# Performance work log

Hardware: AMD Instinct MI355X
Metric: run time of the kernel (lower is better)

The kernel has to match this reference:

```python
import jax, jax.numpy as jnp
import numpy as np
import math

D = 256; NH = 8; NG = 64; META = 6

def _linear(x, w, b):
    return x @ w.T + b

def setup_inputs():
    key = jax.random.key(0)
    ks = jax.random.split(key, 12)
    B, T, TG = 32, 4096, 1024
    def rn(k, shape, s=0.02):
        return jax.random.normal(k, shape, dtype=jnp.float32) * s
    q = jax.random.normal(ks[0], (1, NG, D), dtype=jnp.float32)
    q = q / jnp.clip(jnp.linalg.norm(q, axis=-1, keepdims=True), 1e-6)
    # fibonacci unit sphere anchor, scaled by 0.4
    idx = jnp.arange(NG, dtype=jnp.float32)
    golden = (1.0 + math.sqrt(5.0)) / 2.0
    theta = 2.0 * math.pi * idx / golden
    z = jnp.clip(1.0 - (2.0 * idx + 1.0) / NG, -1.0 + 1e-6, 1.0 - 1e-6)
    r = jnp.sqrt(jnp.clip(1.0 - z * z, 0.0))
    pts = jnp.stack([r * jnp.cos(theta), r * jnp.sin(theta), z], axis=-1)
    pts = pts / jnp.clip(jnp.linalg.norm(pts, axis=-1, keepdims=True), 1e-6)
    p0 = (pts * 0.4)[None]
    ph_b2 = jnp.array([0.0] * 6 + [-2.0] * 4, dtype=jnp.float32)
    return dict(
        local_feat=jax.random.normal(ks[1], (B, D, T), dtype=jnp.float32),
        global_feat=jax.random.normal(ks[2], (B, D, TG), dtype=jnp.float32),
        meta=jax.random.uniform(ks[3], (B, META), dtype=jnp.float32),
        queries=q, p0_anchor=p0,
        in_proj_w=rn(ks[4], (3 * D, D)), in_proj_b=jnp.zeros((3 * D,), jnp.float32),
        out_proj_w=rn(ks[5], (D, D)), out_proj_b=jnp.zeros((D,), jnp.float32),
        ln_g=jnp.ones((D,), jnp.float32), ln_b=jnp.zeros((D,), jnp.float32),
        meta_w=rn(ks[6], (D, META)), meta_b=jnp.zeros((D,), jnp.float32),
        temporal_w=rn(ks[7], (D, D)), temporal_b=jnp.zeros((D,), jnp.float32),
        shift_w=rn(ks[8], (3, D)), shift_b=jnp.zeros((3,), jnp.float32),
        ph_w1=rn(ks[9], (D // 2, D)), ph_b1=jnp.zeros((D // 2,), jnp.float32),
        ph_w2=rn(ks[10], (10, D // 2)), ph_b2=ph_b2,
        wave_delay_scale=jnp.float32(0.1),
        envelope_bias=jnp.float32(0.5),
    )

def reference(local_feat, global_feat, meta, queries, p0_anchor, in_proj_w, in_proj_b,
              out_proj_w, out_proj_b, ln_g, ln_b, meta_w, meta_b, temporal_w, temporal_b,
              shift_w, shift_b, ph_w1, ph_b1, ph_w2, ph_b2, wave_delay_scale, envelope_bias):
    B, _, T = local_feat.shape
    DH = D // NH
    kv = jnp.transpose(global_feat, (0, 2, 1))                        # [B,TG,D]
    q = jnp.broadcast_to(queries, (B, NG, D))
    wq, wk, wv = in_proj_w[:D], in_proj_w[D:2 * D], in_proj_w[2 * D:]
    bq, bk, bv = in_proj_b[:D], in_proj_b[D:2 * D], in_proj_b[2 * D:]
    qh = _linear(q, wq, bq).reshape(B, NG, NH, DH)
    kh = _linear(kv, wk, bk).reshape(B, -1, NH, DH)
    vh = _linear(kv, wv, bv).reshape(B, -1, NH, DH)
    attn = jax.nn.softmax(jnp.einsum('bqhd,bkhd->bhqk', qh, kh) / math.sqrt(DH), axis=-1)
    ctx = jnp.einsum('bhqk,bkhd->bqhd', attn, vh).reshape(B, NG, D)
    x = q + _linear(ctx, out_proj_w, out_proj_b)
    mu = x.mean(-1, keepdims=True)
    var = ((x - mu) ** 2).mean(-1, keepdims=True)
    q_static = (x - mu) / jnp.sqrt(var + 1e-5) * ln_g + ln_b
    q_static = q_static + jax.nn.gelu(_linear(meta, meta_w, meta_b), approximate=False)[:, None, :]
    params = _linear(jax.nn.gelu(_linear(q_static, ph_w1, ph_b1), approximate=False), ph_w2, ph_b2)
    p0_delta = jnp.tanh(params[..., 0:3]) * 0.2
    heart_shift = jnp.tanh(_linear(global_feat.mean(-1), shift_w, shift_b)) * 0.3
    p_pos = p0_anchor + p0_delta + heart_shift[:, None, :]            # [B,NG,3]
    dnorm = jnp.clip(jnp.linalg.norm(params[..., 3:6], axis=-1, keepdims=True), 1e-6)
    dipole_dir = params[..., 3:6] / dnorm
    volume_xyz = jax.nn.sigmoid(params[..., 6:9]) * 0.5 + 0.001
    amplitude = jax.nn.sigmoid(params[..., 9]) + 1e-4                 # [B,NG]
    tw = _linear(q_static, temporal_w, temporal_b)                    # [B,NG,D]
    temporal_logits = jnp.einsum('bnc,bct->bnt', tw, local_feat) / math.sqrt(D)
    idx_sa = jnp.argmax(amplitude, axis=1)                            # [B]
    p_sa = jnp.take_along_axis(p_pos, idx_sa[:, None, None], axis=1)  # [B,1,3]
    dist = jnp.linalg.norm(p_pos - p_sa, axis=-1)                     # [B,NG]
    delay = jnp.clip(jax.nn.softplus(wave_delay_scale) * dist, 0.0, 0.1)
    base_x = jnp.linspace(-1.0, 1.0, T)
    grid_x = base_x[None, None, :] - delay[..., None]                 # [B,NG,T]
    # grid_sample(bilinear, zeros, align_corners=True): grid_y hits rows exactly,
    # so it reduces to 1D linear interp along time with zero padding.
    x_pix = (grid_x + 1.0) * 0.5 * (T - 1)
    x0 = jnp.floor(x_pix).astype(jnp.int32)
    x1 = x0 + 1
    w1 = x_pix - x0.astype(x_pix.dtype)
    w0 = 1.0 - w1
    def samp(xi):
        g = jnp.take_along_axis(temporal_logits, jnp.clip(xi, 0, T - 1), axis=-1)
        return g * ((xi >= 0) & (xi <= T - 1)).astype(g.dtype)
    shifted = w0 * samp(x0) + w1 * samp(x1)
    envelope_t = jax.nn.sigmoid(shifted + envelope_bias)              # [B,NG,T]
    return amplitude, p_pos, dipole_dir, volume_xyz, envelope_t
```

## Files before the change

### kernel.cpp

```cpp
#include <hip/hip_runtime.h>
#include <hip/hip_bf16.h>
#include <math.h>

typedef __hip_bfloat16 bf16;
typedef short s16x8 __attribute__((ext_vector_type(8)));
typedef float f32x4 __attribute__((ext_vector_type(4)));

#define NDIM 256
#define NTG 1024
#define NT 4096

__device__ __forceinline__ float gelu_exact(float x) {
    return 0.5f * x * (1.0f + erff(x * 0.70710678118654752440f));
}
__device__ __forceinline__ float sigmoidf_(float x) {
    return 1.0f / (1.0f + __expf(-x));
}
__device__ __forceinline__ short f2bf_s(float x) {
    union { bf16 h; short s; } cv;
    cv.h = __float2bfloat16(x);
    return cv.s;
}
__device__ __forceinline__ float bf2f(short s) {
    union { bf16 h; short s; } cv;
    cv.s = s;
    return __bfloat162float(cv.h);
}

__global__ __launch_bounds__(256) void k_prep(
        const float* __restrict__ gf, const float* __restrict__ ipw,
        const float* __restrict__ opw, const float* __restrict__ twm,
        const float* __restrict__ pw1, const float* __restrict__ queries,
        const float* __restrict__ ipb,
        bf16* __restrict__ gfT, float* __restrict__ partial,
        float* __restrict__ opwT, float* __restrict__ twT, float* __restrict__ pw1T,
        bf16* __restrict__ wkvK, bf16* __restrict__ wkvV,
        float* __restrict__ qh) {
    __shared__ float smem[64 * 65 + 256];
    int blk = blockIdx.x, tid = threadIdx.x;
    if (blk < 2048) {
        float (*tile)[65] = (float(*)[65])smem;
        float* psum = smem + 64 * 65;
        int t0 = (blk & 15) * 64, c0 = ((blk >> 4) & 3) * 64, b = blk >> 6;
        int tt = tid & 63, ci = tid >> 6;
        #pragma unroll
        for (int r = 0; r < 16; ++r) {
            int cl = ci * 16 + r;
            tile[cl][tt] = gf[((size_t)(b * 256 + c0 + cl)) * NTG + t0 + tt];
        }
        __syncthreads();
        int cc = tid & 63, ti = tid >> 6;
        #pragma unroll
        for (int r = 0; r < 16; ++r) {
            int tl = ti * 16 + r;
            gfT[((size_t)(b * 1024 + t0 + tl)) * 256 + c0 + cc] =
                __float2bfloat16(tile[cc][tl]);
        }
        float ps = 0.f;
        #pragma unroll
        for (int r = 0; r < 16; ++r) ps += tile[cc][ti * 16 + r];
        psum[tid] = ps;
        __syncthreads();
        if (tid < 64) {
            float s = psum[tid] + psum[tid + 64] + psum[tid + 128] + psum[tid + 192];
            partial[(b * 256 + c0 + tid) * 16 + (blk & 15)] = s;
        }
    } else {
        int pblk = blk - 2048;
        if (pblk < 384) {
            int id = pblk * 256 + tid;
            if (id < 65536) {
                int k = id >> 8, c = id & 255;
                opwT[id] = opw[c * 256 + k];
                twT[id]  = twm[c * 256 + k];
            } else {
                int id2 = id - 65536;
                int k = id2 >> 7, m = id2 & 127;
                pw1T[id2] = pw1[m * 256 + k];
            }
        } else if (pblk < 640) {
            int id = (pblk - 384) * 256 + tid;
            wkvK[id] = __float2bfloat16(ipw[65536 + id]);
            wkvV[id] = __float2bfloat16(ipw[131072 + id]);
        } else {
            float* qrow = smem;
            int n = pblk - 640, c = tid;
            qrow[c] = queries[n * 256 + c];
            __syncthreads();
            float s = ipb[c];
            const float* wr = ipw + c * 256;
            for (int k = 0; k < 256; ++k) s += qrow[k] * wr[k];
            qh[n * 256 + c] = s;
        }
    }
}

__global__ __launch_bounds__(256) void k_kv(
        const short* __restrict__ gfT, const short* __restrict__ wkvK,
        const short* __restrict__ wkvV, const float* __restrict__ ipb,
        const float* __restrict__ meta, const float* __restrict__ mw,
        const float* __restrict__ mb, const float* __restrict__ partial,
        const float* __restrict__ sw, const float* __restrict__ sb,
        short* __restrict__ kvh, short* __restrict__ vTg,
        float* __restrict__ metag, float* __restrict__ hshift) {
    int blk = blockIdx.x;
    int tid = threadIdx.x;
    if (blk >= 2048) {
        __shared__ float gm[256];
        int b = blk - 2048, c = tid;
        float m = 0.f;
        const float* pp = partial + (b * 256 + c) * 16;
        #pragma unroll
        for (int tt = 0; tt < 16; ++tt) m += pp[tt];
        gm[c] = m * (1.0f / 1024.0f);
        float s = mb[c];
        #pragma unroll
        for (int j = 0; j < 6; ++j) s += meta[b * 6 + j] * mw[c * 6 + j];
        metag[b * 256 + c] = gelu_exact(s);
        __syncthreads();
        if (c < 3) {
            float t = sb[c];
            for (int k = 0; k < 256; ++k) t += gm[k] * sw[c * 256 + k];
            hshift[b * 4 + c] = tanhf(t) * 0.3f;
        }
        return;
    }
    int w = tid >> 6, lane = tid & 63, lm = lane & 15, quad = lane >> 4;
    int bx = blk & 7, byq = (blk >> 3) & 7, b = blk >> 6;
    int t0 = bx * 128 + w * 32;
    int sel = byq >> 2;
    int n0 = (byq & 3) * 64;
    if (sel == 0) {
        f32x4 acc[4][2];
        #pragma unroll
        for (int ni = 0; ni < 4; ++ni)
            #pragma unroll
            for (int mt = 0; mt < 2; ++mt) acc[ni][mt] = (f32x4)(0.0f);
        #pragma unroll
        for (int ks = 0; ks < 8; ++ks) {
            int c = ks * 32 + quad * 8;
            s16x8 bg[2];
            #pragma unroll
            for (int mt = 0; mt < 2; ++mt)
                bg[mt] = *(const s16x8*)&gfT[((size_t)(b * 1024 + t0 + mt * 16 + lm)) * 256 + c];
            #pragma unroll
            for (int ni = 0; ni < 4; ++ni) {
                s16x8 aw = *(const s16x8*)&wkvK[(n0 + ni * 16 + lm) * 256 + c];
                #pragma unroll
                for (int mt = 0; mt < 2; ++mt)
                    acc[ni][mt] = __builtin_amdgcn_mfma_f32_16x16x32_bf16(aw, bg[mt], acc[ni][mt], 0, 0, 0);
            }
        }
        #pragma unroll
        for (int ni = 0; ni < 4; ++ni) {
            int nb4 = n0 + ni * 16 + quad * 4;
            float4 bias = *(const float4*)&ipb[256 + nb4];
            #pragma unroll
            for (int mt = 0; mt < 2; ++mt) {
                int t = t0 + mt * 16 + lm;
                ushort4 o;
                o.x = (unsigned short)f2bf_s(acc[ni][mt][0] + bias.x);
                o.y = (unsigned short)f2bf_s(acc[ni][mt][1] + bias.y);
                o.z = (unsigned short)f2bf_s(acc[ni][mt][2] + bias.z);
                o.w = (unsigned short)f2bf_s(acc[ni][mt][3] + bias.w);
                *(ushort4*)&kvh[((size_t)(b * 1024 + t)) * 256 + nb4] = o;
            }
        }
    } else {
        f32x4 acc[2][4];
        #pragma unroll
        for (int mt = 0; mt < 2; ++mt)
            #pragma unroll
            for (int ni = 0; ni < 4; ++ni) acc[mt][ni] = (f32x4)(0.0f);
        #pragma unroll
        for (int ks = 0; ks < 8; ++ks) {
            int c = ks * 32 + quad * 8;
            s16x8 ag[2];
            #pragma unroll
            for (int mt = 0; mt < 2; ++mt)
                ag[mt] = *(const s16x8*)&gfT[((size_t)(b * 1024 + t0 + mt * 16 + lm)) * 256 + c];
            #pragma unroll
            for (int ni = 0; ni < 4; ++ni) {
                s16x8 bw = *(const s16x8*)&wkvV[(n0 + ni * 16 + lm) * 256 + c];
                #pragma unroll
                for (int mt = 0; mt < 2; ++mt)
                    acc[mt][ni] = __builtin_amdgcn_mfma_f32_16x16x32_bf16(ag[mt], bw, acc[mt][ni], 0, 0, 0);
            }
        }
        #pragma unroll
        for (int ni = 0; ni < 4; ++ni) {
            int nv = n0 + ni * 16 + lm;
            float bias = ipb[512 + nv];
            #pragma unroll
            for (int mt = 0; mt < 2; ++mt) {
                int t4 = t0 + mt * 16 + quad * 4;
                ushort4 o;
                o.x = (unsigned short)f2bf_s(acc[mt][ni][0] + bias);
                o.y = (unsigned short)f2bf_s(acc[mt][ni][1] + bias);
                o.z = (unsigned short)f2bf_s(acc[mt][ni][2] + bias);
                o.w = (unsigned short)f2bf_s(acc[mt][ni][3] + bias);
                *(ushort4*)&vTg[((size_t)(b * 256 + nv)) * 1024 + t4] = o;
            }
        }
    }
}

__global__ __launch_bounds__(256) void k_attn(
        const short* __restrict__ kvh, const short* __restrict__ vTg,
        const float* __restrict__ qh,
        float* __restrict__ o_half, float* __restrict__ l_half) {
    __shared__ short pT[4][64 * 40];
    __shared__ float obuf[4][64 * 36];
    __shared__ float lbuf[4 * 64];
    int tid = threadIdx.x;
    int w = tid >> 6, lane = tid & 63, lm = lane & 15, quad = lane >> 4;
    int half = blockIdx.x, h = blockIdx.y, b = blockIdx.z;
    s16x8 aq[4];
    #pragma unroll
    for (int mt = 0; mt < 4; ++mt) {
        const float* qp = qh + (mt * 16 + lm) * 256 + h * 32 + quad * 8;
        #pragma unroll
        for (int j = 0; j < 8; ++j) aq[mt][j] = f2bf_s(qp[j]);
    }
    f32x4 acco[2][4];
    #pragma unroll
    for (int dt = 0; dt < 2; ++dt)
        #pragma unroll
        for (int qt = 0; qt < 4; ++qt) acco[dt][qt] = (f32x4)(0.0f);
    float lp[4][4];
    #pragma unroll
    for (int mt = 0; mt < 4; ++mt)
        #pragma unroll
        for (int r = 0; r < 4; ++r) lp[mt][r] = 0.f;
    const float scale = 0.17677669529663687f;
    int kb = half * 512 + w * 128;
    for (int ch = 0; ch < 4; ++ch) {
        int n0 = kb + ch * 32;
        #pragma unroll
        for (int nt = 0; nt < 2; ++nt) {
            int key = n0 + nt * 16 + lm;
            s16x8 bk = *(const s16x8*)&kvh[((size_t)(b * 1024 + key)) * 256 + h * 32 + quad * 8];
            f32x4 zero = {0.f, 0.f, 0.f, 0.f};
            #pragma unroll
            for (int mt = 0; mt < 4; ++mt) {
                f32x4 S = __builtin_amdgcn_mfma_f32_16x16x32_bf16(aq[mt], bk, zero, 0, 0, 0);
                #pragma unroll
                for (int r = 0; r < 4; ++r) {
                    float e = __expf(S[r] * scale);
                    lp[mt][r] += e;
                    pT[w][(mt * 16 + quad * 4 + r) * 40 + nt * 16 + lm] = f2bf_s(e);
                }
            }
        }
        s16x8 av[2], bp[4];
        #pragma unroll
        for (int dt = 0; dt < 2; ++dt)
            av[dt] = *(const s16x8*)&vTg[((size_t)(b * 256 + h * 32 + dt * 16 + lm)) * 1024 + n0 + quad * 8];
        #pragma unroll
        for (int qt = 0; qt < 4; ++qt)
            bp[qt] = *(const s16x8*)&pT[w][(qt * 16 + lm) * 40 + quad * 8];
        #pragma unroll
        for (int dt = 0; dt < 2; ++dt)
            #pragma unroll
            for (int qt = 0; qt < 4; ++qt)
                acco[dt][qt] = __builtin_amdgcn_mfma_f32_16x16x32_bf16(av[dt], bp[qt], acco[dt][qt], 0, 0, 0);
    }
    #pragma unroll
    for (int mt = 0; mt < 4; ++mt)
        #pragma unroll
        for (int r = 0; r < 4; ++r) {
            float v = lp[mt][r];
            v += __shfl_xor(v, 1); v += __shfl_xor(v, 2);
            v += __shfl_xor(v, 4); v += __shfl_xor(v, 8);
            lp[mt][r] = v;
        }
    #pragma unroll
    for (int dt = 0; dt < 2; ++dt)
        #pragma unroll
        for (int qt = 0; qt < 4; ++qt) {
            int q = qt * 16 + lm;
            float4 t;
            t.x = acco[dt][qt][0]; t.y = acco[dt][qt][1];
            t.z = acco[dt][qt][2]; t.w = acco[dt][qt][3];
            *(float4*)&obuf[w][q * 36 + dt * 16 + quad * 4] = t;
        }
    if (lm == 0) {
        #pragma unroll
        for (int mt = 0; mt < 4; ++mt)
            #pragma unroll
            for (int r = 0; r < 4; ++r)
                lbuf[w * 64 + mt * 16 + quad * 4 + r] = lp[mt][r];
    }
    __syncthreads();
    int q = tid & 63, dg = tid >> 6;
    int blk = (b * 8 + h) * 2 + half;
    float l = lbuf[q] + lbuf[64 + q] + lbuf[128 + q] + lbuf[192 + q];
    float o[8];
    #pragma unroll
    for (int j = 0; j < 8; ++j) o[j] = 0.f;
    #pragma unroll
    for (int w2 = 0; w2 < 4; ++w2) {
        const float* src = &obuf[w2][q * 36 + dg * 8];
        #pragma unroll
        for (int j = 0; j < 8; ++j) o[j] += src[j];
    }
    float* dst = &o_half[(((size_t)blk * 64) + q) * 32 + dg * 8];
    #pragma unroll
    for (int j = 0; j < 8; ++j) dst[j] = o[j];
    if (dg == 0) l_half[blk * 64 + q] = l;
}

__global__ __launch_bounds__(256) void k_post(
        const float* __restrict__ o_half, const float* __restrict__ l_half,
        const float* __restrict__ queries,
        const float* __restrict__ opwT, const float* __restrict__ opb,
        const float* __restrict__ lng, const float* __restrict__ lnb,
        const float* __restrict__ metag, const float* __restrict__ hshift,
        const float* __restrict__ twT, const float* __restrict__ tbv,
        const float* __restrict__ pw1T, const float* __restrict__ pb1,
        const float* __restrict__ pw2, const float* __restrict__ pb2,
        const float* __restrict__ p0a,
        bf16* __restrict__ twbf, float* __restrict__ out_amp,
        float* __restrict__ out_ppos, float* __restrict__ out_dip,
        float* __restrict__ out_vol) {
    __shared__ float cs[4][256];
    __shared__ float xs[4][256];
    __shared__ float qs[4][256];
    __shared__ float h1[4][128];
    __shared__ float ps[4][10];
    int tid = threadIdx.x;
    int n0 = blockIdx.x * 4, b = blockIdx.y;
    {
        int h = tid >> 5, d = tid & 31;
        int blk0 = (b * 8 + h) * 2;
        #pragma unroll
        for (int r = 0; r < 4; ++r) {
            int q = n0 + r;
            float l = l_half[blk0 * 64 + q] + l_half[(blk0 + 1) * 64 + q];
            float v0 = o_half[(((size_t)blk0 * 64) + q) * 32 + d];
            float v1 = o_half[(((size_t)(blk0 + 1) * 64) + q) * 32 + d];
            cs[r][tid] = (v0 + v1) / l;
        }
    }
    __syncthreads();
    {
        int c = tid;
        float a[4];
        #pragma unroll
        for (int nn = 0; nn < 4; ++nn) a[nn] = opb[c];
        for (int k = 0; k < 256; ++k) {
            float w = opwT[k * 256 + c];
            #pragma unroll
            for (int nn = 0; nn < 4; ++nn) a[nn] += cs[nn][k] * w;
        }
        #pragma unroll
        for (int nn = 0; nn < 4; ++nn)
            xs[nn][c] = queries[(n0 + nn) * 256 + c] + a[nn];
    }
    __syncthreads();
    {
        int w = tid >> 6, lane = tid & 63;
        int nr = w;
        float x0 = xs[nr][lane], x1 = xs[nr][lane + 64],
              x2 = xs[nr][lane + 128], x3 = xs[nr][lane + 192];
        float s = x0 + x1 + x2 + x3;
        #pragma unroll
        for (int off = 32; off >= 1; off >>= 1) s += __shfl_xor(s, off);
        float mu = s * (1.0f / 256.0f);
        float e0 = x0 - mu, e1 = x1 - mu, e2 = x2 - mu, e3 = x3 - mu;
        float v = e0*e0 + e1*e1 + e2*e2 + e3*e3;
        #pragma unroll
        for (int off = 32; off >= 1; off >>= 1) v += __shfl_xor(v, off);
        float rstd = 1.0f / sqrtf(v * (1.0f / 256.0f) + 1e-5f);
        #pragma unroll
        for (int j = 0; j < 4; ++j) {
            int c = lane + 64 * j;
            qs[nr][c] = (xs[nr][c] - mu) * rstd * lng[c] + lnb[c] + metag[b * 256 + c];
        }
    }
    __syncthreads();
    {
        int c = tid;
        float a[4];
        #pragma unroll
        for (int nn = 0; nn < 4; ++nn) a[nn] = tbv[c];
        for (int k = 0; k < 256; ++k) {
            float w = twT[k * 256 + c];
            #pragma unroll
            for (int nn = 0; nn < 4; ++nn) a[nn] += qs[nn][k] * w;
        }
        #pragma unroll
        for (int nn = 0; nn < 4; ++nn)
            twbf[(size_t)(b * 64 + n0 + nn) * 256 + c] = __float2bfloat16(a[nn]);
    }
    {
        int m = tid & 127, g = tid >> 7;
        float a[2];
        #pragma unroll
        for (int q2 = 0; q2 < 2; ++q2) a[q2] = pb1[m];
        for (int k = 0; k < 256; ++k) {
            float w = pw1T[k * 128 + m];
            #pragma unroll
            for (int q2 = 0; q2 < 2; ++q2) a[q2] += qs[g * 2 + q2][k] * w;
        }
        #pragma unroll
        for (int q2 = 0; q2 < 2; ++q2) h1[g * 2 + q2][m] = gelu_exact(a[q2]);
    }
    __syncthreads();
    if (tid < 40) {
        int nr = tid / 10, j = tid % 10;
        float s = pb2[j];
        for (int m = 0; m < 128; ++m) s += h1[nr][m] * pw2[j * 128 + m];
        ps[nr][j] = s;
    }
    __syncthreads();
    if (tid < 4) {
        int nr = tid;
        int gn = b * 64 + n0 + nr;
        #pragma unroll
        for (int j = 0; j < 3; ++j) {
            float delta = tanhf(ps[nr][j]) * 0.2f;
            out_ppos[gn * 3 + j] = p0a[(n0 + nr) * 3 + j] + delta + hshift[b * 4 + j];
        }
        float d0 = ps[nr][3], d1 = ps[nr][4], d2 = ps[nr][5];
        float dn = fmaxf(sqrtf(d0 * d0 + d1 * d1 + d2 * d2), 1e-6f);
        out_dip[gn * 3 + 0] = d0 / dn;
        out_dip[gn * 3 + 1] = d1 / dn;
        out_dip[gn * 3 + 2] = d2 / dn;
        #pragma unroll
        for (int j = 0; j < 3; ++j)
            out_vol[gn * 3 + j] = sigmoidf_(ps[nr][6 + j]) * 0.5f + 0.001f;
        out_amp[gn] = sigmoidf_(ps[nr][9]) + 0.0001f;
    }
}

__global__ __launch_bounds__(256) void k_temporal(
        const float* __restrict__ lf, const short* __restrict__ twbf,
        short* __restrict__ logits) {
    __shared__ __align__(16) short tws[64 * 264];
    __shared__ __align__(16) short lfs[2][32 * 132];
    int tid = threadIdx.x;
    int t0 = blockIdx.x * 128, b = blockIdx.y;
    int wave = tid >> 6, lane = tid & 63;
    int lm = lane & 15, quad = lane >> 4;

    #pragma unroll
    for (int i = 0; i < 8; ++i) {
        int id = i * 256 + tid;
        int n = id >> 5, c8 = id & 31;
        s16x8 v = *(const s16x8*)&twbf[(size_t)(b * 64 + n) * 256 + c8 * 8];
        *(s16x8*)&tws[n * 264 + c8 * 8] = v;
    }

    float4 fr[4];
    #pragma unroll
    for (int r = 0; r < 4; ++r) {
        int id = r * 256 + tid;
        int c = id >> 5, t4 = id & 31;
        fr[r] = *(const float4*)&lf[((size_t)(b * 256 + c)) * 4096 + t0 + t4 * 4];
    }
    #pragma unroll
    for (int r = 0; r < 4; ++r) {
        int id = r * 256 + tid;
        int c = id >> 5, t4 = id & 31;
        ushort4 o;
        o.x = (unsigned short)f2bf_s(fr[r].x);
        o.y = (unsigned short)f2bf_s(fr[r].y);
        o.z = (unsigned short)f2bf_s(fr[r].z);
        o.w = (unsigned short)f2bf_s(fr[r].w);
        *(ushort4*)&lfs[0][c * 132 + t4 * 4] = o;
    }

    f32x4 acc[2][4];
    #pragma unroll
    for (int mi = 0; mi < 2; ++mi)
        #pragma unroll
        for (int ni = 0; ni < 4; ++ni) acc[mi][ni] = (f32x4)(0.0f);

    __syncthreads();

    for (int ksi = 0; ksi < 8; ++ksi) {
        int cur = ksi & 1;
        if (ksi < 7) {
            int c0n = (ksi + 1) * 32;
            #pragma unroll
            for (int r = 0; r < 4; ++r) {
                int id = r * 256 + tid;
                int c = id >> 5, t4 = id & 31;
                fr[r] = *(const float4*)&lf[((size_t)(b * 256 + c0n + c)) * 4096 + t0 + t4 * 4];
            }
        }
        int c0 = ksi * 32;
        #pragma unroll
        for (int mi = 0; mi < 2; ++mi) {
            int tl = wave * 32 + mi * 16 + lm;
            s16x8 af;
            #pragma unroll
            for (int j = 0; j < 8; ++j)
                af[j] = lfs[cur][(quad * 8 + j) * 132 + tl];
            #pragma unroll
            for (int ni = 0; ni < 4; ++ni) {
                s16x8 bfr = *(const s16x8*)&tws[(ni * 16 + lm) * 264 + c0 + quad * 8];
                acc[mi][ni] = __builtin_amdgcn_mfma_f32_16x16x32_bf16(af, bfr, acc[mi][ni], 0, 0, 0);
            }
        }
        if (ksi < 7) {
            #pragma unroll
            for (int r = 0; r < 4; ++r) {
                int id = r * 256 + tid;
                int c = id >> 5, t4 = id & 31;
                ushort4 o;
                o.x = (unsigned short)f2bf_s(fr[r].x);
                o.y = (unsigned short)f2bf_s(fr[r].y);
                o.z = (unsigned short)f2bf_s(fr[r].z);
                o.w = (unsigned short)f2bf_s(fr[r].w);
                *(ushort4*)&lfs[cur ^ 1][c * 132 + t4 * 4] = o;
            }
        }
        __syncthreads();
    }
    #pragma unroll
    for (int mi = 0; mi < 2; ++mi) {
        #pragma unroll
        for (int ni = 0; ni < 4; ++ni) {
            int n = ni * 16 + lm;
            int t = t0 + wave * 32 + mi * 16 + quad * 4;
            ushort4 o;
            o.x = (unsigned short)f2bf_s(acc[mi][ni][0] * 0.0625f);
            o.y = (unsigned short)f2bf_s(acc[mi][ni][1] * 0.0625f);
            o.z = (unsigned short)f2bf_s(acc[mi][ni][2] * 0.0625f);
            o.w = (unsigned short)f2bf_s(acc[mi][ni][3] * 0.0625f);
            *(ushort4*)&logits[(size_t)(b * 64 + n) * 4096 + t] = o;
        }
    }
}

__global__ void k_envelope(const short* __restrict__ logits,
                           const float* __restrict__ out_amp,
                           const float* __restrict__ out_ppos,
                           const float* __restrict__ wds,
                           const float* __restrict__ ebp,
                           float* __restrict__ env) {
    int blk = blockIdx.x;
    int bn = blk >> 2, seg = blk & 3;
    int b = bn >> 6, n = bn & 63;
    int tid = threadIdx.x;
    int lane = tid & 63;
    float v = out_amp[b * 64 + lane];
    int idx = lane;
    #pragma unroll
    for (int off = 1; off < 64; off <<= 1) {
        float ov = __shfl_xor(v, off);
        int oi = __shfl_xor(idx, off);
        if (ov > v || (ov == v && oi < idx)) { v = ov; idx = oi; }
    }
    float dx = out_ppos[(b * 64 + n) * 3 + 0] - out_ppos[(b * 64 + idx) * 3 + 0];
    float dy = out_ppos[(b * 64 + n) * 3 + 1] - out_ppos[(b * 64 + idx) * 3 + 1];
    float dz = out_ppos[(b * 64 + n) * 3 + 2] - out_ppos[(b * 64 + idx) * 3 + 2];
    float dist = sqrtf(dx * dx + dy * dy + dz * dz);
    float sp = log1pf(expf(wds[0]));
    float dl = fminf(fmaxf(sp * dist, 0.f), 0.1f);
    float eb = ebp[0];
    const short* gl = logits + (size_t)bn * 4096;
    int t_base = seg * 1024 + tid * 4;
    float ov4[4];
    #pragma unroll
    for (int u = 0; u < 4; ++u) {
        int t = t_base + u;
        float xb = fmaf((float)t, 2.0f / 4095.0f, -1.0f);
        float xp = (xb - dl + 1.0f) * 2047.5f;
        float x0f = floorf(xp);
        int x0 = (int)x0f;
        float w1 = xp - x0f, w0 = 1.0f - w1;
        float g0 = (x0 >= 0 && x0 <= 4095) ? bf2f(gl[x0]) : 0.f;
        int x1 = x0 + 1;
        float g1 = (x1 >= 0 && x1 <= 4095) ? bf2f(gl[x1]) : 0.f;
        float sh = w0 * g0 + w1 * g1;
        ov4[u] = 1.0f / (1.0f + __expf(-(sh + eb)));
    }
    float4 o; o.x = ov4[0]; o.y = ov4[1]; o.z = ov4[2]; o.w = ov4[3];
    *reinterpret_cast<float4*>(&env[(size_t)bn * 4096 + t_base]) = o;
}

extern "C" void kernel_launch(void* const* d_in, const int* in_sizes, int n_in,
                              void* d_out, int out_size, void* d_ws, size_t ws_size,
                              hipStream_t stream) {
    const float* lf   = (const float*)d_in[0];
    const float* gf   = (const float*)d_in[1];
    const float* meta = (const float*)d_in[2];
    const float* qrs  = (const float*)d_in[3];
    const float* p0a  = (const float*)d_in[4];
    const float* ipw  = (const float*)d_in[5];
    const float* ipb  = (const float*)d_in[6];
    const float* opw  = (const float*)d_in[7];
    const float* opb  = (const float*)d_in[8];
    const float* lng  = (const float*)d_in[9];
    const float* lnb  = (const float*)d_in[10];
    const float* mw   = (const float*)d_in[11];
    const float* mb   = (const float*)d_in[12];
    const float* twm  = (const float*)d_in[13];
    const float* tbv  = (const float*)d_in[14];
    const float* sw   = (const float*)d_in[15];
    const float* sb   = (const float*)d_in[16];
    const float* pw1  = (const float*)d_in[17];
    const float* pb1  = (const float*)d_in[18];
    const float* pw2  = (const float*)d_in[19];
    const float* pb2  = (const float*)d_in[20];
    const float* wds  = (const float*)d_in[21];
    const float* ebp  = (const float*)d_in[22];

    char* ws = (char*)d_ws;
    short* kvh    = (short*)(ws);
    short* vTg    = (short*)(ws + 16777216);
    short* gfT    = (short*)(ws + 33554432);
    short* logits = (short*)(ws + 50331648);
    float* o_half = (float*)(ws + 67108864);
    float* l_half = (float*)(ws + 71303168);
    short* twbf   = (short*)(ws + 71434240);
    float* qh     = (float*)(ws + 72482816);
    float* metag  = (float*)(ws + 72581120);
    float* hshift = (float*)(ws + 72613888);
    float* opwT   = (float*)(ws + 72614400);
    float* twT    = (float*)(ws + 72876544);
    float* pw1T   = (float*)(ws + 73138688);
    short* wkvK   = (short*)(ws + 73269760);
    short* wkvV   = (short*)(ws + 73400832);
    float* partial= (float*)(ws + 73531904);

    float* out_amp  = (float*)d_out;
    float* out_ppos = out_amp + 2048;
    float* out_dip  = out_amp + 8192;
    float* out_vol  = out_amp + 14336;
    float* env      = out_amp + 20480;

    k_prep<<<2752, 256, 0, stream>>>(gf, ipw, opw, twm, pw1, qrs, ipb,
                                     (bf16*)gfT, partial, opwT, twT, pw1T,
                                     (bf16*)wkvK, (bf16*)wkvV, qh);
    k_kv<<<2080, 256, 0, stream>>>(gfT, wkvK, wkvV, ipb, meta, mw, mb, partial,
                                   sw, sb, kvh, vTg, metag, hshift);
    k_attn<<<dim3(2, 8, 32), 256, 0, stream>>>(kvh, vTg, qh, o_half, l_half);
    k_post<<<dim3(16, 32), 256, 0, stream>>>(o_half, l_half, qrs, opwT, opb, lng, lnb,
                                             metag, hshift, twT, tbv, pw1T, pb1, pw2, pb2,
                                             p0a, (bf16*)twbf, out_amp, out_ppos,
                                             out_dip, out_vol);
    k_temporal<<<dim3(32, 32), 256, 0, stream>>>(lf, twbf, logits);
    k_envelope<<<8192, 256, 0, stream>>>(logits, out_amp, out_ppos, wds, ebp, env);
}
```

Before: 401.8 us.

## Reuse gfT registers across output tiles in k_kv and stage logits in LDS for envelope

k_kv now loads each block's 128x256 slice of gfT into registers once and loops over all four 64-column output tiles, cutting its grid from 2080 to 544 blocks and removing four-fold redundant activation loads. k_envelope now handles a whole (b,n) row per block: it stages the 4096 bf16 logits in zero-padded shared memory, drops the bounds checks on the gathers, and reuses the argmax/delay computation across four segments. The attention kernel's query load is vectorised to float4. Tradeoffs are higher register pressure in k_kv (16 s16x8 operands held live) and fewer blocks, which lowers parallelism.

```diff
diff --git a/kernel.cpp b/kernel.cpp
--- a/kernel.cpp
+++ b/kernel.cpp
@@ -105,9 +105,9 @@
         float* __restrict__ metag, float* __restrict__ hshift) {
     int blk = blockIdx.x;
     int tid = threadIdx.x;
-    if (blk >= 2048) {
+    if (blk >= 512) {
         __shared__ float gm[256];
-        int b = blk - 2048, c = tid;
+        int b = blk - 512, c = tid;
         float m = 0.f;
         const float* pp = partial + (b * 256 + c) * 16;
         #pragma unroll
@@ -126,80 +126,84 @@
         return;
     }
     int w = tid >> 6, lane = tid & 63, lm = lane & 15, quad = lane >> 4;
-    int bx = blk & 7, byq = (blk >> 3) & 7, b = blk >> 6;
+    int bx = blk & 7, sel = (blk >> 3) & 1, b = blk >> 4;
     int t0 = bx * 128 + w * 32;
-    int sel = byq >> 2;
-    int n0 = (byq & 3) * 64;
+    s16x8 g[8][2];
+    #pragma unroll
+    for (int ks = 0; ks < 8; ++ks) {
+        int c = ks * 32 + quad * 8;
+        #pragma unroll
+        for (int mt = 0; mt < 2; ++mt)
+            g[ks][mt] = *(const s16x8*)&gfT[((size_t)(b * 1024 + t0 + mt * 16 + lm)) * 256 + c];
+    }
     if (sel == 0) {
-        f32x4 acc[4][2];
-        #pragma unroll
-        for (int ni = 0; ni < 4; ++ni)
-            #pragma unroll
-            for (int mt = 0; mt < 2; ++mt) acc[ni][mt] = (f32x4)(0.0f);
-        #pragma unroll
-        for (int ks = 0; ks < 8; ++ks) {
-            int c = ks * 32 + quad * 8;
-            s16x8 bg[2];
+        for (int n0i = 0; n0i < 4; ++n0i) {
+            int n0 = n0i * 64;
+            f32x4 acc[4][2];
+            #pragma unroll
+            for (int ni = 0; ni < 4; ++ni)
+                #pragma unroll
+                for (int mt = 0; mt < 2; ++mt) acc[ni][mt] = (f32x4)(0.0f);
+            #pragma unroll
+            for (int ks = 0; ks < 8; ++ks) {
+                int c = ks * 32 + quad * 8;
+                #pragma unroll
+                for (int ni = 0; ni < 4; ++ni) {
+                    s16x8 aw = *(const s16x8*)&wkvK[(n0 + ni * 16 + lm) * 256 + c];
+                    #pragma unroll
+                    for (int mt = 0; mt < 2; ++mt)
+                        acc[ni][mt] = __builtin_amdgcn_mfma_f32_16x16x32_bf16(aw, g[ks][mt], acc[ni][mt], 0, 0, 0);
+                }
+            }
+            #pragma unroll
+            for (int ni = 0; ni < 4; ++ni) {
+                int nb4 = n0 + ni * 16 + quad * 4;
+                float4 bias = *(const float4*)&ipb[256 + nb4];
+                #pragma unroll
+                for (int mt = 0; mt < 2; ++mt) {
+                    int t = t0 + mt * 16 + lm;
+                    ushort4 o;
+                    o.x = (unsigned short)f2bf_s(acc[ni][mt][0] + bias.x);
+                    o.y = (unsigned short)f2bf_s(acc[ni][mt][1] + bias.y);
+                    o.z = (unsigned short)f2bf_s(acc[ni][mt][2] + bias.z);
+                    o.w = (unsigned short)f2bf_s(acc[ni][mt][3] + bias.w);
+                    *(ushort4*)&kvh[((size_t)(b * 1024 + t)) * 256 + nb4] = o;
+                }
+            }
+        }
+    } else {
+        for (int n0i = 0; n0i < 4; ++n0i) {
+            int n0 = n0i * 64;
+            f32x4 acc[2][4];
             #pragma unroll
             for (int mt = 0; mt < 2; ++mt)
-                bg[mt] = *(const s16x8*)&gfT[((size_t)(b * 1024 + t0 + mt * 16 + lm)) * 256 + c];
+                #pragma unroll
+                for (int ni = 0; ni < 4; ++ni) acc[mt][ni] = (f32x4)(0.0f);
+            #pragma unroll
+            for (int ks = 0; ks < 8; ++ks) {
+                int c = ks * 32 + quad * 8;
+                #pragma unroll
+                for (int ni = 0; ni < 4; ++ni) {
+                    s16x8 bw = *(const s16x8*)&wkvV[(n0 + ni * 16 + lm) * 256 + c];
+                    #pragma unroll
+                    for (int mt = 0; mt < 2; ++mt)
+                        acc[mt][ni] = __builtin_amdgcn_mfma_f32_16x16x32_bf16(g[ks][mt], bw, acc[mt][ni], 0, 0, 0);
+                }
+            }
             #pragma unroll
             for (int ni = 0; ni < 4; ++ni) {
-                s16x8 aw = *(const s16x8*)&wkvK[(n0 + ni * 16 + lm) * 256 + c];
+                int nv = n0 + ni * 16 + lm;
+                float bias = ipb[512 + nv];
                 #pragma unroll
-                for (int mt = 0; mt < 2; ++mt)
-                    acc[ni][mt] = __builtin_amdgcn_mfma_f32_16x16x32_bf16(aw, bg[mt], acc[ni][mt], 0, 0, 0);
-            }
-        }
-        #pragma unroll
-        for (int ni = 0; ni < 4; ++ni) {
-            int nb4 = n0 + ni * 16 + quad * 4;
-            float4 bias = *(const float4*)&ipb[256 + nb4];
-            #pragma unroll
-            for (int mt = 0; mt < 2; ++mt) {
-                int t = t0 + mt * 16 + lm;
-                ushort4 o;
-                o.x = (unsigned short)f2bf_s(acc[ni][mt][0] + bias.x);
-                o.y = (unsigned short)f2bf_s(acc[ni][mt][1] + bias.y);
-                o.z = (unsigned short)f2bf_s(acc[ni][mt][2] + bias.z);
-                o.w = (unsigned short)f2bf_s(acc[ni][mt][3] + bias.w);
-                *(ushort4*)&kvh[((size_t)(b * 1024 + t)) * 256 + nb4] = o;
-            }
-        }
-    } else {
-        f32x4 acc[2][4];
-        #pragma unroll
-        for (int mt = 0; mt < 2; ++mt)
-            #pragma unroll
-            for (int ni = 0; ni < 4; ++ni) acc[mt][ni] = (f32x4)(0.0f);
-        #pragma unroll
-        for (int ks = 0; ks < 8; ++ks) {
-            int c = ks * 32 + quad * 8;
-            s16x8 ag[2];
-            #pragma unroll
-            for (int mt = 0; mt < 2; ++mt)
-                ag[mt] = *(const s16x8*)&gfT[((size_t)(b * 1024 + t0 + mt * 16 + lm)) * 256 + c];
-            #pragma unroll
-            for (int ni = 0; ni < 4; ++ni) {
-                s16x8 bw = *(const s16x8*)&wkvV[(n0 + ni * 16 + lm) * 256 + c];
-                #pragma unroll
-                for (int mt = 0; mt < 2; ++mt)
-                    acc[mt][ni] = __builtin_amdgcn_mfma_f32_16x16x32_bf16(ag[mt], bw, acc[mt][ni], 0, 0, 0);
-            }
-        }
-        #pragma unroll
-        for (int ni = 0; ni < 4; ++ni) {
-            int nv = n0 + ni * 16 + lm;
-            float bias = ipb[512 + nv];
-            #pragma unroll
-            for (int mt = 0; mt < 2; ++mt) {
-                int t4 = t0 + mt * 16 + quad * 4;
-                ushort4 o;
-                o.x = (unsigned short)f2bf_s(acc[mt][ni][0] + bias);
-                o.y = (unsigned short)f2bf_s(acc[mt][ni][1] + bias);
-                o.z = (unsigned short)f2bf_s(acc[mt][ni][2] + bias);
-                o.w = (unsigned short)f2bf_s(acc[mt][ni][3] + bias);
-                *(ushort4*)&vTg[((size_t)(b * 256 + nv)) * 1024 + t4] = o;
+                for (int mt = 0; mt < 2; ++mt) {
+                    int t4 = t0 + mt * 16 + quad * 4;
+                    ushort4 o;
+                    o.x = (unsigned short)f2bf_s(acc[mt][ni][0] + bias);
+                    o.y = (unsigned short)f2bf_s(acc[mt][ni][1] + bias);
+                    o.z = (unsigned short)f2bf_s(acc[mt][ni][2] + bias);
+                    o.w = (unsigned short)f2bf_s(acc[mt][ni][3] + bias);
+                    *(ushort4*)&vTg[((size_t)(b * 256 + nv)) * 1024 + t4] = o;
+                }
             }
         }
     }
@@ -218,9 +222,12 @@
     s16x8 aq[4];
     #pragma unroll
     for (int mt = 0; mt < 4; ++mt) {
-        const float* qp = qh + (mt * 16 + lm) * 256 + h * 32 + quad * 8;
-        #pragma unroll
-        for (int j = 0; j < 8; ++j) aq[mt][j] = f2bf_s(qp[j]);
+        const float4* qp = (const float4*)(qh + (mt * 16 + lm) * 256 + h * 32 + quad * 8);
+        float4 qa = qp[0], qb = qp[1];
+        aq[mt][0] = f2bf_s(qa.x); aq[mt][1] = f2bf_s(qa.y);
+        aq[mt][2] = f2bf_s(qa.z); aq[mt][3] = f2bf_s(qa.w);
+        aq[mt][4] = f2bf_s(qb.x); aq[mt][5] = f2bf_s(qb.y);
+        aq[mt][6] = f2bf_s(qb.z); aq[mt][7] = f2bf_s(qb.w);
     }
     f32x4 acco[2][4];
     #pragma unroll
@@ -535,17 +542,27 @@
     }
 }
 
-__global__ void k_envelope(const short* __restrict__ logits,
-                           const float* __restrict__ out_amp,
-                           const float* __restrict__ out_ppos,
-                           const float* __restrict__ wds,
-                           const float* __restrict__ ebp,
-                           float* __restrict__ env) {
-    int blk = blockIdx.x;
-    int bn = blk >> 2, seg = blk & 3;
+__global__ __launch_bounds__(256) void k_envelope(
+        const short* __restrict__ logits,
+        const float* __restrict__ out_amp,
+        const float* __restrict__ out_ppos,
+        const float* __restrict__ wds,
+        const float* __restrict__ ebp,
+        float* __restrict__ env) {
+    __shared__ __align__(16) short ls[208 + 4096 + 16];
+    int bn = blockIdx.x;
     int b = bn >> 6, n = bn & 63;
     int tid = threadIdx.x;
     int lane = tid & 63;
+    if (tid < 208) ls[tid] = 0;
+    if (tid < 16) ls[208 + 4096 + tid] = 0;
+    const short* gl = logits + (size_t)bn * 4096;
+    {
+        s16x8 v0 = *(const s16x8*)&gl[tid * 16];
+        s16x8 v1 = *(const s16x8*)&gl[tid * 16 + 8];
+        *(s16x8*)&ls[208 + tid * 16] = v0;
+        *(s16x8*)&ls[208 + tid * 16 + 8] = v1;
+    }
     float v = out_amp[b * 64 + lane];
     int idx = lane;
     #pragma unroll
@@ -561,25 +578,27 @@
     float sp = log1pf(expf(wds[0]));
     float dl = fminf(fmaxf(sp * dist, 0.f), 0.1f);
     float eb = ebp[0];
-    const short* gl = logits + (size_t)bn * 4096;
-    int t_base = seg * 1024 + tid * 4;
-    float ov4[4];
-    #pragma unroll
-    for (int u = 0; u < 4; ++u) {
-        int t = t_base + u;
-        float xb = fmaf((float)t, 2.0f / 4095.0f, -1.0f);
-        float xp = (xb - dl + 1.0f) * 2047.5f;
-        float x0f = floorf(xp);
-        int x0 = (int)x0f;
-        float w1 = xp - x0f, w0 = 1.0f - w1;
-        float g0 = (x0 >= 0 && x0 <= 4095) ? bf2f(gl[x0]) : 0.f;
-        int x1 = x0 + 1;
-        float g1 = (x1 >= 0 && x1 <= 4095) ? bf2f(gl[x1]) : 0.f;
-        float sh = w0 * g0 + w1 * g1;
-        ov4[u] = 1.0f / (1.0f + __expf(-(sh + eb)));
-    }
-    float4 o; o.x = ov4[0]; o.y = ov4[1]; o.z = ov4[2]; o.w = ov4[3];
-    *reinterpret_cast<float4*>(&env[(size_t)bn * 4096 + t_base]) = o;
+    __syncthreads();
+    #pragma unroll
+    for (int g = 0; g < 4; ++g) {
+        int t_base = g * 1024 + tid * 4;
+        float ov4[4];
+        #pragma unroll
+        for (int u = 0; u < 4; ++u) {
+            int t = t_base + u;
+            float xb = fmaf((float)t, 2.0f / 4095.0f, -1.0f);
+            float xp = (xb - dl + 1.0f) * 2047.5f;
+            float x0f = floorf(xp);
+            int x0 = (int)x0f;
+            float w1 = xp - x0f, w0 = 1.0f - w1;
+            float g0 = bf2f(ls[208 + x0]);
+            float g1 = bf2f(ls[208 + x0 + 1]);
+            float sh = w0 * g0 + w1 * g1;
+            ov4[u] = 1.0f / (1.0f + __expf(-(sh + eb)));
+        }
+        float4 o; o.x = ov4[0]; o.y = ov4[1]; o.z = ov4[2]; o.w = ov4[3];
+        *reinterpret_cast<float4*>(&env[(size_t)bn * 4096 + t_base]) = o;
+    }
 }
 
 extern "C" void kernel_launch(void* const* d_in, const int* in_sizes, int n_in,
@@ -636,13 +655,13 @@
     k_prep<<<2752, 256, 0, stream>>>(gf, ipw, opw, twm, pw1, qrs, ipb,
                                      (bf16*)gfT, partial, opwT, twT, pw1T,
                                      (bf16*)wkvK, (bf16*)wkvV, qh);
-    k_kv<<<2080, 256, 0, stream>>>(gfT, wkvK, wkvV, ipb, meta, mw, mb, partial,
-                                   sw, sb, kvh, vTg, metag, hshift);
+    k_kv<<<544, 256, 0, stream>>>(gfT, wkvK, wkvV, ipb, meta, mw, mb, partial,
+                                  sw, sb, kvh, vTg, metag, hshift);
     k_attn<<<dim3(2, 8, 32), 256, 0, stream>>>(kvh, vTg, qh, o_half, l_half);
     k_post<<<dim3(16, 32), 256, 0, stream>>>(o_half, l_half, qrs, opwT, opb, lng, lnb,
                                              metag, hshift, twT, tbv, pw1T, pb1, pw2, pb2,
                                              p0a, (bf16*)twbf, out_amp, out_ppos,
                                              out_dip, out_vol);
     k_temporal<<<dim3(32, 32), 256, 0, stream>>>(lf, twbf, logits);
-    k_envelope<<<8192, 256, 0, stream>>>(logits, out_amp, out_ppos, wds, ebp, env);
-}
+    k_envelope<<<2048, 256, 0, stream>>>(logits, out_amp, out_ppos, wds, ebp, env);
+}
```

Measured after the change: 389.0 us. 1.03x faster.
